# Kernel optimization log

Measured on AMD Instinct MI355X. Metric: run time of the kernel, lower is better.

Reference implementation:

```python
import jax, jax.numpy as jnp
import numpy as np

NB = 5  # number of graph nodes per image
COUNT_THRESH = 10000  # min pixel count for a region to be selected
BOX_DOWNSCALE = 16.0  # backbone stride


def _masks_to_boxes(mask_np, ids):
    # torchvision.ops.masks_to_boxes: (xmin, ymin, xmax, ymax) in pixel coords
    boxes = []
    for oid in ids:
        ys, xs = np.nonzero(mask_np == oid)
        boxes.append([xs.min(), ys.min(), xs.max(), ys.max()])
    return np.asarray(boxes, dtype=np.float32)


def _select_boxes(seg_logits):
    # mask = espnet(x).max(1)[1]; original code only keeps boxes from the LAST
    # batch element (loop variable overwritten each iteration) -- preserved here.
    mask = np.asarray(jnp.argmax(seg_logits, axis=1))[-1]
    ids, counts = np.unique(mask, return_counts=True)
    ids, counts = ids[1:], counts[1:]  # drop background / first label
    boxes = _masks_to_boxes(mask, ids) / BOX_DOWNSCALE  # feature-map coords
    # rr = argsort(argsort(counts, descending)) == rank of each region by size
    rr = np.argsort(np.argsort(-counts))
    sel = []
    for idx in range(len(boxes)):
        for b_idx in range(len(rr)):
            if idx == rr[b_idx] and counts[b_idx] > COUNT_THRESH and len(sel) < NB - 2:
                sel.append(b_idx)
                break
    return boxes.astype(np.int64), sel


def setup_inputs() -> dict:
    key = jax.random.key(0)
    k1, k2, k3 = jax.random.split(key, 3)
    N, K, Hin, Win = 4, 20, 480, 640   # even H/W -> parity padding is a no-op
    C, H, W = 512, Hin // 16, Win // 16  # stride-16 VGG backbone features
    return {
        "seg_logits": jax.random.normal(k1, (N, K, Hin, Win), jnp.float32),
        "feat": jax.random.normal(k2, (N, C, H, W), jnp.float32),
        "pool_x": jax.random.normal(k3, (N, C), jnp.float32),
    }


def reference(seg_logits, feat, pool_x):
    boxes, sel = _select_boxes(seg_logits)
    N, C, H, W = feat.shape
    # Selected-region crops; boxes identical for every batch element (original
    # bug), so each crop+resize is vectorized over the batch dim.
    nodes = []
    for b in sel:
        x0, y0, x1, y1 = [int(v) for v in boxes[b]]
        crop = feat[:, :, y0:y1, x0:x1]
        nodes.append(jax.image.resize(crop, (N, C, H, W), "bilinear"))
    # Fixed fallback boxes (center, left/top/right/bottom strips)
    bb = [[W // 4, H // 4, 3 * W // 4, 3 * H // 4],
          [0, 0, W // 3, H],
          [0, 0, W, H // 3],
          [2 * W // 3, 0, W, H],
          [0, 2 * H // 3, W, H]]
    if len(nodes) < NB:
        for i in range(len(bb) - len(nodes)):  # range evaluated once, as in original
            x0, y0, x1, y1 = bb[i]
            crop = feat[:, :, y0:y1, x0:x1]
            nodes.append(jax.image.resize(crop, (N, C, H, W), "bilinear"))
    graph_nodes = jnp.stack(nodes, axis=1)  # [N, NB, C, H, W]
    # Original: graph_nodes.view(NB, N, ...) is a raw reshape, then cat with feat
    x_cropped = jnp.concatenate(
        [graph_nodes.reshape(NB, N, C, H, W), feat[None]], axis=0)  # [NB+1,N,C,H,W]
    return pool_x, NB, N, x_cropped
```

## Files before the change

kernel.cpp:

```cpp
#include <hip/hip_runtime.h>
#include <hip/hip_bf16.h>

#define K_CLS 20
#define HIN 480
#define WIN 640
#define NPIX (HIN * WIN)
#define C_ 512
#define H_ 30
#define W_ 40
#define HW_ (H_ * W_)
#define NB_ 5
#define CNT_THRESH 10000
#define XCROP_ELEMS (6 * 4 * C_ * H_ * W_)
#define ELEMS_PER_SN (C_ * H_ * W_)
#define OUT_TOTAL (2050 + XCROP_ELEMS)

#define NBLK_STATS 300

typedef float f32x2 __attribute__((ext_vector_type(2)));
typedef float f32x4 __attribute__((ext_vector_type(4)));

#define F_CPB 4
#define F_CGRP (C_ / F_CPB)
#define F_TPB 512
#define F_BLOCKS (4 * F_CGRP)


__global__ void stats_k(const float* __restrict__ seg, int* __restrict__ ws) {
    __shared__ int s_cnt[K_CLS], s_mnx[K_CLS], s_mny[K_CLS], s_mxx[K_CLS], s_mxy[K_CLS];
    int t = threadIdx.x;
    if (t < K_CLS) { s_cnt[t] = 0; s_mnx[t] = WIN; s_mny[t] = HIN; s_mxx[t] = -1; s_mxy[t] = -1; }
    __syncthreads();

    int p = blockIdx.x * blockDim.x + t;
    const float4* base = (const float4*)(seg + (size_t)3 * K_CLS * NPIX) + p;
    float4 v = base[0];
    float b0 = v.x, b1 = v.y, b2 = v.z, b3 = v.w;
    int k0 = 0, k1 = 0, k2 = 0, k3 = 0;
    #pragma unroll
    for (int k = 1; k < K_CLS; k++) {
        float4 u = base[(size_t)k * (NPIX / 4)];
        if (u.x > b0) { b0 = u.x; k0 = k; }
        if (u.y > b1) { b1 = u.y; k1 = k; }
        if (u.z > b2) { b2 = u.z; k2 = k; }
        if (u.w > b3) { b3 = u.w; k3 = k; }
    }
    int x = (p * 4) % WIN, y = (p * 4) / WIN;
    if (k0 == k1 && k1 == k2 && k2 == k3) {
        atomicAdd(&s_cnt[k0], 4);
        atomicMin(&s_mnx[k0], x);     atomicMax(&s_mxx[k0], x + 3);
        atomicMin(&s_mny[k0], y);     atomicMax(&s_mxy[k0], y);
    } else {
        int ks[4] = {k0, k1, k2, k3};
        #pragma unroll
        for (int i = 0; i < 4; i++) {
            atomicAdd(&s_cnt[ks[i]], 1);
            atomicMin(&s_mnx[ks[i]], x + i);  atomicMax(&s_mxx[ks[i]], x + i);
            atomicMin(&s_mny[ks[i]], y);      atomicMax(&s_mxy[ks[i]], y);
        }
    }
    __syncthreads();
    if (t < 100) {
        int a = t / 20, c = t % 20;
        int val = (a == 0) ? s_cnt[c] : (a == 1) ? s_mnx[c] : (a == 2) ? s_mny[c]
                : (a == 3) ? s_mxx[c] : s_mxy[c];
        ws[blockIdx.x * 100 + t] = val;
    }
}

__global__ __launch_bounds__(F_TPB) void fuse_k(const float* __restrict__ feat,
                      const int* __restrict__ ws,
                      const float* __restrict__ pool_x,
                      float* __restrict__ out) {
    __shared__ float sf[F_CPB * HW_];
    __shared__ int part[5][100];
    __shared__ int st[100];
    __shared__ int s_nb[NB_ * 4];

    int t  = threadIdx.x;
    int n  = blockIdx.x / F_CGRP;
    int c0 = (blockIdx.x % F_CGRP) * F_CPB;

    const float* src = feat + ((size_t)n * C_ + c0) * HW_;
    float* cdst = out + 2050 + (size_t)(20 + n) * ELEMS_PER_SN + (size_t)c0 * HW_;
    for (int i = t; i < (F_CPB * HW_) / 4; i += F_TPB) {
        f32x4 v = ((const f32x4*)src)[i];
        ((f32x4*)sf)[i] = v;
        f32x2 lo = {v.x, v.y}, hi = {v.z, v.w};
        __builtin_nontemporal_store(lo, (f32x2*)(cdst + i * 4));
        __builtin_nontemporal_store(hi, (f32x2*)(cdst + i * 4 + 2));
    }
    if (blockIdx.x == 0) {
        for (int i = t; i < 1024; i += F_TPB)
            ((float2*)out)[i] = ((const float2*)pool_x)[i];
        if (t == 0) { out[2048] = 5.0f; out[2049] = 4.0f; }
    }

    if (t < 500) {
        int c = t % 100, chunk = t / 100;
        int a = c / 20;
        int acc = (a == 0) ? 0 : (a == 1) ? WIN : (a == 2) ? HIN : -1;
        #pragma unroll
        for (int i = 0; i < 60; i++) {
            int v = ws[(chunk * 60 + i) * 100 + c];
            if (a == 0)      acc += v;
            else if (a <= 2) acc = min(acc, v);
            else             acc = max(acc, v);
        }
        part[chunk][c] = acc;
    }
    __syncthreads();
    if (t < 100) {
        int a = t / 20;
        int acc = part[0][t];
        #pragma unroll
        for (int i = 1; i < 5; i++) {
            int v = part[i][t];
            if (a == 0)      acc += v;
            else if (a <= 2) acc = min(acc, v);
            else             acc = max(acc, v);
        }
        st[t] = acc;
    }
    __syncthreads();

    if (t < 64) {
        int k = t;
        bool valid = k < K_CLS;
        int ck = valid ? st[k] : 0;
        bool present = valid && ck > 0;
        unsigned long long pmask = __ballot(present);
        int firstp = __ffsll((long long)pmask) - 1;
        bool cand = present && (k != firstp);
        bool pass = cand && ck > CNT_THRESH;

        int rank = 0;
        #pragma unroll
        for (int j = 0; j < K_CLS; j++) {
            int cj = st[j];
            bool candj = (cj > 0) && (j != firstp);
            if (candj && (cj > ck || (cj == ck && j < k))) rank++;
        }
        int selpos = 0;
        #pragma unroll
        for (int j = 0; j < K_CLS; j++) {
            int rj = __shfl(rank, j, 64);
            int pj = __shfl((int)pass, j, 64);
            if (pj && rj < rank) selpos++;
        }
        bool selected = pass && selpos < (NB_ - 2);
        if (selected) {
            s_nb[selpos * 4 + 0] = st[20 + k] >> 4;
            s_nb[selpos * 4 + 1] = st[40 + k] >> 4;
            s_nb[selpos * 4 + 2] = st[60 + k] >> 4;
            s_nb[selpos * 4 + 3] = st[80 + k] >> 4;
        }
        int nsel = __popcll(__ballot(selected));
        #define BBW(i, A, B, Cc, D) \
            if (t == nsel + i && t < NB_) { \
                s_nb[t * 4 + 0] = A; s_nb[t * 4 + 1] = B; \
                s_nb[t * 4 + 2] = Cc; s_nb[t * 4 + 3] = D; }
        BBW(0, W_ / 4, H_ / 4, 3 * W_ / 4, 3 * H_ / 4)
        BBW(1, 0, 0, W_ / 3, H_)
        BBW(2, 0, 0, W_, H_ / 3)
        BBW(3, 2 * W_ / 3, 0, W_, H_)
        BBW(4, 0, 2 * H_ / 3, W_, H_)
        #undef BBW
    }
    __syncthreads();

    for (int b = 0; b < NB_; b++) {
        int x0 = s_nb[b * 4 + 0], y0 = s_nb[b * 4 + 1];
        int x1 = s_nb[b * 4 + 2], y1 = s_nb[b * 4 + 3];
        int iw = max(x1 - x0, 1), ih = max(y1 - y0, 1);
        int cb = y0 * W_ + x0;
        float sx = (float)iw * (1.0f / (float)W_);
        float sy = (float)ih * (1.0f / (float)H_);
        float* ob = out + 2050 + (size_t)(5 * n + b) * ELEMS_PER_SN + (size_t)c0 * HW_;

        for (int hw = t; hw < HW_; hw += F_TPB) {
            int h = hw / W_;
            int w = hw - h * W_;

            float fy  = ((float)h + 0.5f) * sy - 0.5f;
            float flY = floorf(fy);
            float ty  = fy - flY;
            int ylo_u = (int)flY;
            int ylo = max(ylo_u, 0);
            int yhi = min(ylo_u + 1, ih - 1);

            float fx  = ((float)w + 0.5f) * sx - 0.5f;
            float flX = floorf(fx);
            float tx  = fx - flX;
            int xlo_u = (int)flX;
            int xlo = max(xlo_u, 0);
            int xhi = min(xlo_u + 1, iw - 1);

            int i00 = cb + ylo * W_ + xlo, i01 = cb + ylo * W_ + xhi;
            int i10 = cb + yhi * W_ + xlo, i11 = cb + yhi * W_ + xhi;

            float* op = ob + hw;
            #pragma unroll
            for (int j = 0; j < F_CPB; j++) {
                const float* sp = sf + j * HW_;
                float v00 = sp[i00], v01 = sp[i01];
                float v10 = sp[i10], v11 = sp[i11];
                float top = v00 + tx * (v01 - v00);
                float bot = v10 + tx * (v11 - v10);
                __builtin_nontemporal_store(top + ty * (bot - top), op + j * HW_);
            }
        }
    }
}

extern "C" void kernel_launch(void* const* d_in, const int* in_sizes, int n_in,
                              void* d_out, int out_size, void* d_ws, size_t ws_size,
                              hipStream_t stream) {
    const float* seg    = (const float*)d_in[0];
    const float* feat   = (const float*)d_in[1];
    const float* pool_x = (const float*)d_in[2];
    float* out = (float*)d_out;
    int* ws = (int*)d_ws;

    stats_k<<<NBLK_STATS, 256, 0, stream>>>(seg, ws);
    fuse_k<<<F_BLOCKS, F_TPB, 0, stream>>>(feat, ws, pool_x, out);
}
```

Baseline: 183.2 us.

## Compute box plan once in a single-block kernel instead of per block

```diff
diff --git a/kernel.cpp b/kernel.cpp
--- a/kernel.cpp
+++ b/kernel.cpp
@@ -16,6 +16,7 @@
 #define OUT_TOTAL (2050 + XCROP_ELEMS)
 
 #define NBLK_STATS 300
+#define NODE_OFF (NBLK_STATS * 100)
 
 typedef float f32x2 __attribute__((ext_vector_type(2)));
 typedef float f32x4 __attribute__((ext_vector_type(4)));
@@ -68,18 +69,99 @@
     }
 }
 
+__global__ void plan_k(int* __restrict__ ws, const float* __restrict__ pool_x,
+                       float* __restrict__ out) {
+    __shared__ int part[10][100];
+    __shared__ int st[100];
+    int t = threadIdx.x;
+
+    ((float2*)out)[t] = ((const float2*)pool_x)[t];
+    if (t == 0) { out[2048] = 5.0f; out[2049] = 4.0f; }
+
+    if (t < 1000) {
+        int c = t % 100, chunk = t / 100;
+        int a = c / 20;
+        int acc = (a == 0) ? 0 : (a == 1) ? WIN : (a == 2) ? HIN : -1;
+        #pragma unroll
+        for (int i = 0; i < 30; i++) {
+            int v = ws[(chunk * 30 + i) * 100 + c];
+            if (a == 0)      acc += v;
+            else if (a <= 2) acc = min(acc, v);
+            else             acc = max(acc, v);
+        }
+        part[chunk][c] = acc;
+    }
+    __syncthreads();
+    if (t < 100) {
+        int a = t / 20;
+        int acc = part[0][t];
+        #pragma unroll
+        for (int i = 1; i < 10; i++) {
+            int v = part[i][t];
+            if (a == 0)      acc += v;
+            else if (a <= 2) acc = min(acc, v);
+            else             acc = max(acc, v);
+        }
+        st[t] = acc;
+    }
+    __syncthreads();
+
+    if (t < 64) {
+        int k = t;
+        bool valid = k < K_CLS;
+        int ck = valid ? st[k] : 0;
+        bool present = valid && ck > 0;
+        unsigned long long pmask = __ballot(present);
+        int firstp = __ffsll((long long)pmask) - 1;
+        bool pass = present && (k != firstp) && ck > CNT_THRESH;
+
+        int rank = 0;
+        #pragma unroll
+        for (int j = 0; j < K_CLS; j++) {
+            int cj = st[j];
+            bool candj = (cj > 0) && (j != firstp);
+            if (candj && (cj > ck || (cj == ck && j < k))) rank++;
+        }
+        int selpos = 0;
+        #pragma unroll
+        for (int j = 0; j < K_CLS; j++) {
+            int rj = __shfl(rank, j, 64);
+            int pj = __shfl((int)pass, j, 64);
+            if (pj && rj < rank) selpos++;
+        }
+        bool selected = pass && selpos < (NB_ - 2);
+        int* nb = ws + NODE_OFF;
+        if (selected) {
+            nb[selpos * 4 + 0] = st[20 + k] >> 4;
+            nb[selpos * 4 + 1] = st[40 + k] >> 4;
+            nb[selpos * 4 + 2] = st[60 + k] >> 4;
+            nb[selpos * 4 + 3] = st[80 + k] >> 4;
+        }
+        int nsel = __popcll(__ballot(selected));
+        #define BBW(i, A, B, Cc, D) \
+            if (t == nsel + i && t < NB_) { \
+                nb[t * 4 + 0] = A; nb[t * 4 + 1] = B; \
+                nb[t * 4 + 2] = Cc; nb[t * 4 + 3] = D; }
+        BBW(0, W_ / 4, H_ / 4, 3 * W_ / 4, 3 * H_ / 4)
+        BBW(1, 0, 0, W_ / 3, H_)
+        BBW(2, 0, 0, W_, H_ / 3)
+        BBW(3, 2 * W_ / 3, 0, W_, H_)
+        BBW(4, 0, 2 * H_ / 3, W_, H_)
+        #undef BBW
+    }
+}
+
 __global__ __launch_bounds__(F_TPB) void fuse_k(const float* __restrict__ feat,
-                      const int* __restrict__ ws,
-                      const float* __restrict__ pool_x,
+                      const int* __restrict__ nb,
                       float* __restrict__ out) {
     __shared__ float sf[F_CPB * HW_];
-    __shared__ int part[5][100];
-    __shared__ int st[100];
     __shared__ int s_nb[NB_ * 4];
 
     int t  = threadIdx.x;
     int n  = blockIdx.x / F_CGRP;
     int c0 = (blockIdx.x % F_CGRP) * F_CPB;
+
+    if (t < NB_ * 4) s_nb[t] = nb[t];
 
     const float* src = feat + ((size_t)n * C_ + c0) * HW_;
     float* cdst = out + 2050 + (size_t)(20 + n) * ELEMS_PER_SN + (size_t)c0 * HW_;
@@ -89,83 +171,6 @@
         f32x2 lo = {v.x, v.y}, hi = {v.z, v.w};
         __builtin_nontemporal_store(lo, (f32x2*)(cdst + i * 4));
         __builtin_nontemporal_store(hi, (f32x2*)(cdst + i * 4 + 2));
-    }
-    if (blockIdx.x == 0) {
-        for (int i = t; i < 1024; i += F_TPB)
-            ((float2*)out)[i] = ((const float2*)pool_x)[i];
-        if (t == 0) { out[2048] = 5.0f; out[2049] = 4.0f; }
-    }
-
-    if (t < 500) {
-        int c = t % 100, chunk = t / 100;
-        int a = c / 20;
-        int acc = (a == 0) ? 0 : (a == 1) ? WIN : (a == 2) ? HIN : -1;
-        #pragma unroll
-        for (int i = 0; i < 60; i++) {
-            int v = ws[(chunk * 60 + i) * 100 + c];
-            if (a == 0)      acc += v;
-            else if (a <= 2) acc = min(acc, v);
-            else             acc = max(acc, v);
-        }
-        part[chunk][c] = acc;
-    }
-    __syncthreads();
-    if (t < 100) {
-        int a = t / 20;
-        int acc = part[0][t];
-        #pragma unroll
-        for (int i = 1; i < 5; i++) {
-            int v = part[i][t];
-            if (a == 0)      acc += v;
-            else if (a <= 2) acc = min(acc, v);
-            else             acc = max(acc, v);
-        }
-        st[t] = acc;
-    }
-    __syncthreads();
-
-    if (t < 64) {
-        int k = t;
-        bool valid = k < K_CLS;
-        int ck = valid ? st[k] : 0;
-        bool present = valid && ck > 0;
-        unsigned long long pmask = __ballot(present);
-        int firstp = __ffsll((long long)pmask) - 1;
-        bool cand = present && (k != firstp);
-        bool pass = cand && ck > CNT_THRESH;
-
-        int rank = 0;
-        #pragma unroll
-        for (int j = 0; j < K_CLS; j++) {
-            int cj = st[j];
-            bool candj = (cj > 0) && (j != firstp);
-            if (candj && (cj > ck || (cj == ck && j < k))) rank++;
-        }
-        int selpos = 0;
-        #pragma unroll
-        for (int j = 0; j < K_CLS; j++) {
-            int rj = __shfl(rank, j, 64);
-            int pj = __shfl((int)pass, j, 64);
-            if (pj && rj < rank) selpos++;
-        }
-        bool selected = pass && selpos < (NB_ - 2);
-        if (selected) {
-            s_nb[selpos * 4 + 0] = st[20 + k] >> 4;
-            s_nb[selpos * 4 + 1] = st[40 + k] >> 4;
-            s_nb[selpos * 4 + 2] = st[60 + k] >> 4;
-            s_nb[selpos * 4 + 3] = st[80 + k] >> 4;
-        }
-        int nsel = __popcll(__ballot(selected));
-        #define BBW(i, A, B, Cc, D) \
-            if (t == nsel + i && t < NB_) { \
-                s_nb[t * 4 + 0] = A; s_nb[t * 4 + 1] = B; \
-                s_nb[t * 4 + 2] = Cc; s_nb[t * 4 + 3] = D; }
-        BBW(0, W_ / 4, H_ / 4, 3 * W_ / 4, 3 * H_ / 4)
-        BBW(1, 0, 0, W_ / 3, H_)
-        BBW(2, 0, 0, W_, H_ / 3)
-        BBW(3, 2 * W_ / 3, 0, W_, H_)
-        BBW(4, 0, 2 * H_ / 3, W_, H_)
-        #undef BBW
     }
     __syncthreads();
 
@@ -223,5 +228,6 @@
     int* ws = (int*)d_ws;
 
     stats_k<<<NBLK_STATS, 256, 0, stream>>>(seg, ws);
-    fuse_k<<<F_BLOCKS, F_TPB, 0, stream>>>(feat, ws, pool_x, out);
-}
+    plan_k<<<1, 1024, 0, stream>>>(ws, pool_x, out);
+    fuse_k<<<F_BLOCKS, F_TPB, 0, stream>>>(feat, ws + NODE_OFF, out);
+}
```

After: 180.3 us. About the same (-1.6%).
